# Performance work log

Measured on AMD Instinct MI355X. Metric: run time of the kernel, lower is better.

## Reference

```python
import jax, jax.numpy as jnp
import numpy as np

EPSILON = 1e-10
NUM_STATES = 16
EPS_POT = 1.0
DIFFUSION = 3
N_NODES = 100000
N_UND_EDGES = 1600000
FEAT_DIM = 128


def setup_inputs() -> dict:
    key = jax.random.key(0)
    k1, k2, k3, k4 = jax.random.split(key, 4)
    features = jax.random.normal(k1, (N_NODES, FEAT_DIM), dtype=jnp.float32)
    W = jax.random.normal(k2, (FEAT_DIM, NUM_STATES), dtype=jnp.float32) * 0.05
    u = jax.random.randint(k3, (N_UND_EDGES,), 0, N_NODES)
    v = jax.random.randint(k4, (N_UND_EDGES,), 0, N_NODES)
    # directed edge lists: each undirected edge appears in both directions
    src_nodes = jnp.concatenate([u, v])
    dst_nodes = jnp.concatenate([v, u])
    e = jnp.arange(N_UND_EDGES)
    rev_edges = jnp.concatenate([e + N_UND_EDGES, e])  # index of reversed edge
    return {
        "features": features,
        "W": W,
        "src_nodes": src_nodes,
        "dst_nodes": dst_nodes,
        "rev_edges": rev_edges,
    }


def reference(features, W, src_nodes, dst_nodes, rev_edges):
    num_dir_edges = src_nodes.shape[0]
    potential = jnp.exp(jnp.eye(NUM_STATES, dtype=features.dtype) * EPS_POT)
    # classifier: linear + softmax -> probability priors [N, S]
    priors = jax.nn.softmax(features @ W, axis=1)
    log_priors = jnp.log(jnp.maximum(priors, EPSILON))

    beliefs = priors
    messages = jnp.full((num_dir_edges, NUM_STATES), 1.0 / NUM_STATES,
                        dtype=features.dtype)
    for _ in range(DIFFUSION):
        # message update: gather-divide-matmul-renormalize
        new_beliefs = beliefs[src_nodes]          # [2E, S]
        rev_messages = messages[rev_edges]        # [2E, S]
        new_msgs = (new_beliefs / rev_messages) @ potential
        messages = new_msgs / new_msgs.sum(axis=1, keepdims=True)
        # belief update: scatter-add of log messages, then softmax
        log_msgs = jnp.log(jnp.maximum(messages, EPSILON))
        log_b = log_priors.at[dst_nodes].add(log_msgs)
        beliefs = jax.nn.softmax(log_b, axis=1)
    return (priors, beliefs)
```

## Files before the change

### kernel.cpp

```cpp
#include <hip/hip_runtime.h>
#include <hip/hip_fp16.h>

#define NSTATES 16
#define P_PART 4
#define C_CHUNK 32

static __device__ __forceinline__ float4 ld4(const float* p) {
    return *reinterpret_cast<const float4*>(p);
}

struct h4 { __half2 a, b; };

static __device__ __forceinline__ float4 ldh4(const __half* p) {
    h4 v = *reinterpret_cast<const h4*>(p);
    float2 fa = __half22float2(v.a);
    float2 fb = __half22float2(v.b);
    return make_float4(fa.x, fa.y, fb.x, fb.y);
}
static __device__ __forceinline__ void sth4(__half* p, float4 f) {
    h4 v;
    v.a = __floats2half2_rn(f.x, f.y);
    v.b = __floats2half2_rn(f.z, f.w);
    *reinterpret_cast<h4*>(p) = v;
}

__global__ void priors_kernel(const float* __restrict__ feat,
                              const float* __restrict__ W,
                              float* __restrict__ priors_out,
                              float* __restrict__ beliefs,
                              float* __restrict__ log_priors,
                              int n_nodes)
{
    __shared__ float Wl[128 * NSTATES];
    for (int i = threadIdx.x; i < 128 * NSTATES; i += blockDim.x)
        Wl[i] = W[i];
    __syncthreads();

    long long gid = (long long)blockIdx.x * blockDim.x + threadIdx.x;
    int node = (int)(gid >> 4);
    if (node >= n_nodes) return;
    int s = (int)(gid & 15);

    const float4* f4 = reinterpret_cast<const float4*>(feat + (size_t)node * 128);
    float acc = 0.f;
#pragma unroll
    for (int i = 0; i < 32; ++i) {
        float4 f = f4[i];
        acc = fmaf(f.x, Wl[(i * 4 + 0) * NSTATES + s], acc);
        acc = fmaf(f.y, Wl[(i * 4 + 1) * NSTATES + s], acc);
        acc = fmaf(f.z, Wl[(i * 4 + 2) * NSTATES + s], acc);
        acc = fmaf(f.w, Wl[(i * 4 + 3) * NSTATES + s], acc);
    }
    float mx = acc;
#pragma unroll
    for (int off = 1; off < 16; off <<= 1)
        mx = fmaxf(mx, __shfl_xor(mx, off, 64));
    float ex = expf(acc - mx);
    float sm = ex;
#pragma unroll
    for (int off = 1; off < 16; off <<= 1)
        sm += __shfl_xor(sm, off, 64);
    float p = ex / sm;

    size_t idx = (size_t)node * NSTATES + s;
    priors_out[idx] = p;
    beliefs[idx]    = p;
    log_priors[idx] = logf(fmaxf(p, 1e-10f));
}

__global__ void __launch_bounds__(1024) hist1_kernel(
    const int* __restrict__ dst, int* __restrict__ percount,
    int n, int n_nodes, int bins, int chunk)
{
    extern __shared__ int lh[];
    int c = blockIdx.x & (C_CHUNK - 1);
    int p = blockIdx.x / C_CHUNK;
    int base = p * bins;
    for (int i = threadIdx.x; i < bins; i += 1024) lh[i] = 0;
    __syncthreads();
    int lo = c * chunk, hi = min(lo + chunk, n);
    for (int i = lo + threadIdx.x; i < hi; i += 1024) {
        int d = dst[i] - base;
        if ((unsigned)d < (unsigned)bins) atomicAdd(&lh[d], 1);
    }
    __syncthreads();
    int lim = min(bins, n_nodes - base);
    int* out = percount + (size_t)c * n_nodes + base;
    for (int i = threadIdx.x; i < lim; i += 1024) out[i] = lh[i];
}

__global__ void colscan_kernel(int* __restrict__ percount,
                               int* __restrict__ cnt, int n_nodes)
{
    int v = blockIdx.x * blockDim.x + threadIdx.x;
    if (v >= n_nodes) return;
    int acc = 0;
#pragma unroll
    for (int c = 0; c < C_CHUNK; ++c) {
        size_t idx = (size_t)c * n_nodes + v;
        int x = percount[idx];
        percount[idx] = acc;
        acc += x;
    }
    cnt[v] = acc;
}

__global__ void scan1_kernel(const int* __restrict__ cnt,
                             int* __restrict__ row_ptr,
                             int* __restrict__ bsum, int n)
{
    int base = blockIdx.x * 1024;
    int t = threadIdx.x;
    int i0 = base + t * 4;
    int a0 = (i0 + 0 < n) ? cnt[i0 + 0] : 0;
    int a1 = (i0 + 1 < n) ? cnt[i0 + 1] : 0;
    int a2 = (i0 + 2 < n) ? cnt[i0 + 2] : 0;
    int a3 = (i0 + 3 < n) ? cnt[i0 + 3] : 0;
    int sl = a0 + a1 + a2 + a3;

    int lane = t & 63, wid = t >> 6;
    int v = sl;
#pragma unroll
    for (int off = 1; off < 64; off <<= 1) {
        int tv = __shfl_up(v, off, 64);
        if (lane >= off) v += tv;
    }
    __shared__ int wtot[4], woff[4];
    if (lane == 63) wtot[wid] = v;
    __syncthreads();
    if (t == 0) {
        int a = 0;
        for (int w = 0; w < 4; ++w) { woff[w] = a; a += wtot[w]; }
        bsum[blockIdx.x] = a;
    }
    __syncthreads();
    int excl = woff[wid] + (v - sl);
    if (i0 + 0 < n) row_ptr[i0 + 0] = excl;
    if (i0 + 1 < n) row_ptr[i0 + 1] = excl + a0;
    if (i0 + 2 < n) row_ptr[i0 + 2] = excl + a0 + a1;
    if (i0 + 3 < n) row_ptr[i0 + 3] = excl + a0 + a1 + a2;
}

__global__ void scan2_kernel(int* __restrict__ bsum, int nb)
{
    __shared__ int run;
    int lane = threadIdx.x;
    if (lane == 0) run = 0;
    __syncthreads();
    for (int b = 0; b < nb; b += 64) {
        int i = b + lane;
        int x = (i < nb) ? bsum[i] : 0;
        int v = x;
#pragma unroll
        for (int off = 1; off < 64; off <<= 1) {
            int tv = __shfl_up(v, off, 64);
            if (lane >= off) v += tv;
        }
        int excl = run + v - x;
        if (i < nb) bsum[i] = excl;
        __syncthreads();
        if (lane == 63) run = excl + x;
        __syncthreads();
    }
}

__global__ void scan3_kernel(int* __restrict__ row_ptr,
                             const int* __restrict__ bsum, int n, int total)
{
    int i = blockIdx.x * blockDim.x + threadIdx.x;
    if (i < n) row_ptr[i] += bsum[i >> 10];
    if (i == 0) row_ptr[n] = total;
}

__global__ void __launch_bounds__(1024) slot3_kernel(
    const int* __restrict__ dst, const int* __restrict__ row_ptr,
    const int* __restrict__ percount, int* __restrict__ slot_of,
    int n, int n_nodes, int bins, int chunk)
{
    extern __shared__ int lh[];
    int c = blockIdx.x & (C_CHUNK - 1);
    int p = blockIdx.x / C_CHUNK;
    int base = p * bins;
    for (int i = threadIdx.x; i < bins; i += 1024) lh[i] = 0;
    __syncthreads();
    int lo = c * chunk, hi = min(lo + chunk, n);
    const int* pc = percount + (size_t)c * n_nodes;
    for (int i = lo + threadIdx.x; i < hi; i += 1024) {
        int d = dst[i];
        int ld = d - base;
        if ((unsigned)ld < (unsigned)bins) {
            int lr = atomicAdd(&lh[ld], 1);
            slot_of[i] = row_ptr[d] + pc[d] + lr;
        }
    }
}

template <bool FIRST>
__global__ void edge_kernel(const float* __restrict__ beliefs,
                            __half* __restrict__ messages,
                            const int* __restrict__ src,
                            const int* __restrict__ dst,
                            const int* __restrict__ slot_of,
                            int n_pairs)
{
    long long gid = (long long)blockIdx.x * blockDim.x + threadIdx.x;
    int p = (int)(gid >> 2);
    if (p >= n_pairs) return;
    int sub = (int)(gid & 3);

    int u  = src[p];
    int v  = dst[p];
    int sF = slot_of[p];
    int sR = slot_of[p + n_pairs];

    const float EM1  = 1.7182818284590452354f;
    const float SUMF = 17.718281828459045235f;

    float4 bu = ld4(beliefs + (size_t)u * NSTATES + sub * 4);
    float4 bv = ld4(beliefs + (size_t)v * NSTATES + sub * 4);

    float4 tf, tr;
    if (FIRST) {
        tf = make_float4(bu.x * 16.f, bu.y * 16.f, bu.z * 16.f, bu.w * 16.f);
        tr = make_float4(bv.x * 16.f, bv.y * 16.f, bv.z * 16.f, bv.w * 16.f);
    } else {
        float4 mf = ldh4(messages + (size_t)sF * NSTATES + sub * 4);
        float4 mr = ldh4(messages + (size_t)sR * NSTATES + sub * 4);
        tf = make_float4(bu.x / mr.x, bu.y / mr.y, bu.z / mr.z, bu.w / mr.w);
        tr = make_float4(bv.x / mf.x, bv.y / mf.y, bv.z / mf.z, bv.w / mf.w);
    }

    float sf = (tf.x + tf.y) + (tf.z + tf.w);
    float sr = (tr.x + tr.y) + (tr.z + tr.w);
    sf += __shfl_xor(sf, 1, 64);
    sf += __shfl_xor(sf, 2, 64);
    sr += __shfl_xor(sr, 1, 64);
    sr += __shfl_xor(sr, 2, 64);

    float invf = 1.0f / (SUMF * sf);
    float invr = 1.0f / (SUMF * sr);

    float4 nf, nr;
    nf.x = fmaf(EM1, tf.x, sf) * invf;
    nf.y = fmaf(EM1, tf.y, sf) * invf;
    nf.z = fmaf(EM1, tf.z, sf) * invf;
    nf.w = fmaf(EM1, tf.w, sf) * invf;
    nr.x = fmaf(EM1, tr.x, sr) * invr;
    nr.y = fmaf(EM1, tr.y, sr) * invr;
    nr.z = fmaf(EM1, tr.z, sr) * invr;
    nr.w = fmaf(EM1, tr.w, sr) * invr;

    sth4(messages + (size_t)sF * NSTATES + sub * 4, nf);
    sth4(messages + (size_t)sR * NSTATES + sub * 4, nr);
}

__global__ void belief_kernel(const __half* __restrict__ messages,
                              const int* __restrict__ row_ptr,
                              const float* __restrict__ log_priors,
                              float* __restrict__ beliefs,
                              int n_nodes)
{
    long long gid = (long long)blockIdx.x * blockDim.x + threadIdx.x;
    int node = (int)(gid >> 6);
    if (node >= n_nodes) return;
    int lane = threadIdx.x & 63;
    int cp   = lane & 7;
    int rg   = lane >> 3;

    int start = row_ptr[node];
    int end   = row_ptr[node + 1];

    float acc0 = 0.f, acc1 = 0.f;
    for (int row = start + rg; row < end; row += 8) {
        __half2 m2 = *reinterpret_cast<const __half2*>(
            messages + (size_t)row * NSTATES + cp * 2);
        float2 f = __half22float2(m2);
        acc0 += logf(fmaxf(f.x, 1e-10f));
        acc1 += logf(fmaxf(f.y, 1e-10f));
    }
#pragma unroll
    for (int off = 8; off < 64; off <<= 1) {
        acc0 += __shfl_xor(acc0, off, 64);
        acc1 += __shfl_xor(acc1, off, 64);
    }

    float2 lp = *reinterpret_cast<const float2*>(
        log_priors + (size_t)node * NSTATES + cp * 2);
    float lb0 = acc0 + lp.x;
    float lb1 = acc1 + lp.y;

    float mx = fmaxf(lb0, lb1);
#pragma unroll
    for (int off = 1; off < 8; off <<= 1)
        mx = fmaxf(mx, __shfl_xor(mx, off, 64));
    float e0 = expf(lb0 - mx);
    float e1 = expf(lb1 - mx);
    float sm = e0 + e1;
#pragma unroll
    for (int off = 1; off < 8; off <<= 1)
        sm += __shfl_xor(sm, off, 64);
    float inv = 1.0f / sm;

    if (rg == 0) {
        float2 b = make_float2(e0 * inv, e1 * inv);
        *reinterpret_cast<float2*>(beliefs + (size_t)node * NSTATES + cp * 2) = b;
    }
}

extern "C" void kernel_launch(void* const* d_in, const int* in_sizes, int n_in,
                              void* d_out, int out_size, void* d_ws, size_t ws_size,
                              hipStream_t stream)
{
    const float* feat = (const float*)d_in[0];
    const float* W    = (const float*)d_in[1];
    const int*   src  = (const int*)d_in[2];
    const int*   dst  = (const int*)d_in[3];

    int n_nodes = in_sizes[0] / 128;
    int n_dir   = in_sizes[2];
    int n_pairs = n_dir / 2;

    float* out         = (float*)d_out;
    float* priors_out  = out;
    float* beliefs     = out + (size_t)n_nodes * NSTATES;

    size_t NN16 = (size_t)n_nodes * NSTATES;
    size_t ME   = (size_t)n_dir * NSTATES;

    float*  ws         = (float*)d_ws;
    float*  log_priors = ws;
    __half* messages   = (__half*)(log_priors + NN16);
    int*    slot_of    = (int*)(messages + ME);
    int*    row_ptr    = slot_of + n_dir;
    int*    cnt        = row_ptr + n_nodes + 1;
    int*    bsum       = cnt + n_nodes;
    int*    percount   = bsum + ((n_nodes + 1023) / 1024) + 1;

    const int BLK = 256;
    int nb    = (n_nodes + 1023) / 1024;
    int bins  = (n_nodes + P_PART - 1) / P_PART;
    int chunk = (n_dir + C_CHUNK - 1) / C_CHUNK;
    int grid1 = (int)((NN16 + BLK - 1) / BLK);
    int gridE = (int)(((size_t)n_pairs * 4 + BLK - 1) / BLK);
    int gridN = (n_nodes + BLK - 1) / BLK;
    int gridB = (int)(((size_t)n_nodes * 64 + BLK - 1) / BLK);

    hist1_kernel<<<P_PART * C_CHUNK, 1024, bins * sizeof(int), stream>>>(
        dst, percount, n_dir, n_nodes, bins, chunk);
    colscan_kernel<<<gridN, BLK, 0, stream>>>(percount, cnt, n_nodes);
    scan1_kernel<<<nb, 256, 0, stream>>>(cnt, row_ptr, bsum, n_nodes);
    scan2_kernel<<<1, 64, 0, stream>>>(bsum, nb);
    scan3_kernel<<<gridN, BLK, 0, stream>>>(row_ptr, bsum, n_nodes, n_dir);
    slot3_kernel<<<P_PART * C_CHUNK, 1024, bins * sizeof(int), stream>>>(
        dst, row_ptr, percount, slot_of, n_dir, n_nodes, bins, chunk);

    priors_kernel<<<grid1, BLK, 0, stream>>>(feat, W, priors_out, beliefs,
                                             log_priors, n_nodes);

    edge_kernel<true><<<gridE, BLK, 0, stream>>>(beliefs, messages, src, dst,
                                                 slot_of, n_pairs);
    belief_kernel<<<gridB, BLK, 0, stream>>>(messages, row_ptr, log_priors,
                                             beliefs, n_nodes);

    edge_kernel<false><<<gridE, BLK, 0, stream>>>(beliefs, messages, src, dst,
                                                  slot_of, n_pairs);
    belief_kernel<<<gridB, BLK, 0, stream>>>(messages, row_ptr, log_priors,
                                             beliefs, n_nodes);

    edge_kernel<false><<<gridE, BLK, 0, stream>>>(beliefs, messages, src, dst,
                                                  slot_of, n_pairs);
    belief_kernel<<<gridB, BLK, 0, stream>>>(messages, row_ptr, log_priors,
                                             beliefs, n_nodes);
}
```

Measured before the change: 760.5 us.

## Fuse belief and message updates into a dst-sorted node kernel with reverse-slot map

```diff
diff --git a/kernel.cpp b/kernel.cpp
--- a/kernel.cpp
+++ b/kernel.cpp
@@ -5,30 +5,13 @@
 #define P_PART 4
 #define C_CHUNK 32
 
-static __device__ __forceinline__ float4 ld4(const float* p) {
-    return *reinterpret_cast<const float4*>(p);
-}
-
-struct h4 { __half2 a, b; };
-
-static __device__ __forceinline__ float4 ldh4(const __half* p) {
-    h4 v = *reinterpret_cast<const h4*>(p);
-    float2 fa = __half22float2(v.a);
-    float2 fb = __half22float2(v.b);
-    return make_float4(fa.x, fa.y, fb.x, fb.y);
-}
-static __device__ __forceinline__ void sth4(__half* p, float4 f) {
-    h4 v;
-    v.a = __floats2half2_rn(f.x, f.y);
-    v.b = __floats2half2_rn(f.z, f.w);
-    *reinterpret_cast<h4*>(p) = v;
-}
-
 __global__ void priors_kernel(const float* __restrict__ feat,
                               const float* __restrict__ W,
                               float* __restrict__ priors_out,
-                              float* __restrict__ beliefs,
                               float* __restrict__ log_priors,
+                              const int* __restrict__ srev,
+                              const int* __restrict__ row_ptr,
+                              __half* __restrict__ msgs_out,
                               int n_nodes)
 {
     __shared__ float Wl[128 * NSTATES];
@@ -64,8 +47,18 @@
 
     size_t idx = (size_t)node * NSTATES + s;
     priors_out[idx] = p;
-    beliefs[idx]    = p;
     log_priors[idx] = logf(fmaxf(p, 1e-10f));
+
+    const float EM1  = 1.7182818284590452354f;
+    const float SUMF = 17.718281828459045235f;
+    __half h = __float2half((1.f + EM1 * p) * (1.f / SUMF));
+
+    int start = row_ptr[node];
+    int end   = row_ptr[node + 1];
+    for (int r = start; r < end; ++r) {
+        int tgt = srev[r];
+        msgs_out[(size_t)tgt * NSTATES + s] = h;
+    }
 }
 
 __global__ void __launch_bounds__(1024) hist1_kernel(
@@ -195,115 +188,81 @@
     }
 }
 
-template <bool FIRST>
-__global__ void edge_kernel(const float* __restrict__ beliefs,
-                            __half* __restrict__ messages,
-                            const int* __restrict__ src,
-                            const int* __restrict__ dst,
-                            const int* __restrict__ slot_of,
-                            int n_pairs)
-{
-    long long gid = (long long)blockIdx.x * blockDim.x + threadIdx.x;
-    int p = (int)(gid >> 2);
-    if (p >= n_pairs) return;
-    int sub = (int)(gid & 3);
-
-    int u  = src[p];
-    int v  = dst[p];
-    int sF = slot_of[p];
-    int sR = slot_of[p + n_pairs];
-
-    const float EM1  = 1.7182818284590452354f;
-    const float SUMF = 17.718281828459045235f;
-
-    float4 bu = ld4(beliefs + (size_t)u * NSTATES + sub * 4);
-    float4 bv = ld4(beliefs + (size_t)v * NSTATES + sub * 4);
-
-    float4 tf, tr;
-    if (FIRST) {
-        tf = make_float4(bu.x * 16.f, bu.y * 16.f, bu.z * 16.f, bu.w * 16.f);
-        tr = make_float4(bv.x * 16.f, bv.y * 16.f, bv.z * 16.f, bv.w * 16.f);
-    } else {
-        float4 mf = ldh4(messages + (size_t)sF * NSTATES + sub * 4);
-        float4 mr = ldh4(messages + (size_t)sR * NSTATES + sub * 4);
-        tf = make_float4(bu.x / mr.x, bu.y / mr.y, bu.z / mr.z, bu.w / mr.w);
-        tr = make_float4(bv.x / mf.x, bv.y / mf.y, bv.z / mf.z, bv.w / mf.w);
-    }
-
-    float sf = (tf.x + tf.y) + (tf.z + tf.w);
-    float sr = (tr.x + tr.y) + (tr.z + tr.w);
-    sf += __shfl_xor(sf, 1, 64);
-    sf += __shfl_xor(sf, 2, 64);
-    sr += __shfl_xor(sr, 1, 64);
-    sr += __shfl_xor(sr, 2, 64);
-
-    float invf = 1.0f / (SUMF * sf);
-    float invr = 1.0f / (SUMF * sr);
-
-    float4 nf, nr;
-    nf.x = fmaf(EM1, tf.x, sf) * invf;
-    nf.y = fmaf(EM1, tf.y, sf) * invf;
-    nf.z = fmaf(EM1, tf.z, sf) * invf;
-    nf.w = fmaf(EM1, tf.w, sf) * invf;
-    nr.x = fmaf(EM1, tr.x, sr) * invr;
-    nr.y = fmaf(EM1, tr.y, sr) * invr;
-    nr.z = fmaf(EM1, tr.z, sr) * invr;
-    nr.w = fmaf(EM1, tr.w, sr) * invr;
-
-    sth4(messages + (size_t)sF * NSTATES + sub * 4, nf);
-    sth4(messages + (size_t)sR * NSTATES + sub * 4, nr);
-}
-
-__global__ void belief_kernel(const __half* __restrict__ messages,
-                              const int* __restrict__ row_ptr,
-                              const float* __restrict__ log_priors,
-                              float* __restrict__ beliefs,
-                              int n_nodes)
+__global__ void __launch_bounds__(1024) srev_kernel(
+    const int* __restrict__ slot_of, const int* __restrict__ row_ptr,
+    int* __restrict__ srev, int n, int n_pairs, int n_nodes, int bins, int chunk)
+{
+    int c = blockIdx.x & (C_CHUNK - 1);
+    int p = blockIdx.x / C_CHUNK;
+    int nlo = p * bins;
+    int nhi = min(nlo + bins, n_nodes);
+    int slo = row_ptr[nlo];
+    int shi = row_ptr[nhi];
+    int lo = c * chunk, hi = min(lo + chunk, n);
+    for (int i = lo + threadIdx.x; i < hi; i += 1024) {
+        int s = slot_of[i];
+        if (s >= slo && s < shi) {
+            int r = (i < n_pairs) ? i + n_pairs : i - n_pairs;
+            srev[s] = slot_of[r];
+        }
+    }
+}
+
+template <bool WRITE_MSGS, bool WRITE_B>
+__global__ void fused_kernel(const __half* __restrict__ min_,
+                             __half* __restrict__ mout,
+                             const int* __restrict__ srev,
+                             const int* __restrict__ row_ptr,
+                             const float* __restrict__ log_priors,
+                             float* __restrict__ beliefs_out,
+                             int n_nodes)
 {
     long long gid = (long long)blockIdx.x * blockDim.x + threadIdx.x;
     int node = (int)(gid >> 6);
     if (node >= n_nodes) return;
     int lane = threadIdx.x & 63;
-    int cp   = lane & 7;
-    int rg   = lane >> 3;
+    int j = lane & 15;
+    int g = lane >> 4;
 
     int start = row_ptr[node];
     int end   = row_ptr[node + 1];
 
-    float acc0 = 0.f, acc1 = 0.f;
-    for (int row = start + rg; row < end; row += 8) {
-        __half2 m2 = *reinterpret_cast<const __half2*>(
-            messages + (size_t)row * NSTATES + cp * 2);
-        float2 f = __half22float2(m2);
-        acc0 += logf(fmaxf(f.x, 1e-10f));
-        acc1 += logf(fmaxf(f.y, 1e-10f));
-    }
-#pragma unroll
-    for (int off = 8; off < 64; off <<= 1) {
-        acc0 += __shfl_xor(acc0, off, 64);
-        acc1 += __shfl_xor(acc1, off, 64);
-    }
-
-    float2 lp = *reinterpret_cast<const float2*>(
-        log_priors + (size_t)node * NSTATES + cp * 2);
-    float lb0 = acc0 + lp.x;
-    float lb1 = acc1 + lp.y;
-
-    float mx = fmaxf(lb0, lb1);
-#pragma unroll
-    for (int off = 1; off < 8; off <<= 1)
+    float acc = 0.f;
+    for (int row = start + g; row < end; row += 4)
+        acc += logf(__half2float(min_[(size_t)row * NSTATES + j]));
+    acc += __shfl_xor(acc, 16, 64);
+    acc += __shfl_xor(acc, 32, 64);
+
+    float lb = acc + log_priors[(size_t)node * NSTATES + j];
+    float mx = lb;
+#pragma unroll
+    for (int off = 1; off < 16; off <<= 1)
         mx = fmaxf(mx, __shfl_xor(mx, off, 64));
-    float e0 = expf(lb0 - mx);
-    float e1 = expf(lb1 - mx);
-    float sm = e0 + e1;
-#pragma unroll
-    for (int off = 1; off < 8; off <<= 1)
+    float e_ = expf(lb - mx);
+    float sm = e_;
+#pragma unroll
+    for (int off = 1; off < 16; off <<= 1)
         sm += __shfl_xor(sm, off, 64);
-    float inv = 1.0f / sm;
-
-    if (rg == 0) {
-        float2 b = make_float2(e0 * inv, e1 * inv);
-        *reinterpret_cast<float2*>(beliefs + (size_t)node * NSTATES + cp * 2) = b;
+    float b = e_ / sm;
+
+    if (WRITE_B && g == 0)
+        beliefs_out[(size_t)node * NSTATES + j] = b;
+
+    if (WRITE_MSGS) {
+        const float EM1  = 1.7182818284590452354f;
+        const float SUMF = 17.718281828459045235f;
+        for (int row = start + g; row < end; row += 4) {
+            float m = __half2float(min_[(size_t)row * NSTATES + j]);
+            float t = b / m;
+            float s = t;
+            s += __shfl_xor(s, 1, 64);
+            s += __shfl_xor(s, 2, 64);
+            s += __shfl_xor(s, 4, 64);
+            s += __shfl_xor(s, 8, 64);
+            float out = fmaf(EM1, t, s) * (1.0f / (SUMF * s));
+            int tgt = srev[row];
+            mout[(size_t)tgt * NSTATES + j] = __float2half(out);
+        }
     }
 }
 
@@ -313,7 +272,6 @@
 {
     const float* feat = (const float*)d_in[0];
     const float* W    = (const float*)d_in[1];
-    const int*   src  = (const int*)d_in[2];
     const int*   dst  = (const int*)d_in[3];
 
     int n_nodes = in_sizes[0] / 128;
@@ -322,26 +280,28 @@
 
     float* out         = (float*)d_out;
     float* priors_out  = out;
-    float* beliefs     = out + (size_t)n_nodes * NSTATES;
+    float* beliefs_out = out + (size_t)n_nodes * NSTATES;
 
     size_t NN16 = (size_t)n_nodes * NSTATES;
     size_t ME   = (size_t)n_dir * NSTATES;
 
-    float*  ws         = (float*)d_ws;
-    float*  log_priors = ws;
-    __half* messages   = (__half*)(log_priors + NN16);
-    int*    slot_of    = (int*)(messages + ME);
-    int*    row_ptr    = slot_of + n_dir;
-    int*    cnt        = row_ptr + n_nodes + 1;
-    int*    bsum       = cnt + n_nodes;
-    int*    percount   = bsum + ((n_nodes + 1023) / 1024) + 1;
+    char* base = (char*)d_ws;
+    __half* bufA       = (__half*)base;
+    __half* bufB       = (__half*)(base + ME * sizeof(__half));
+    float*  log_priors = (float*)(base + 2 * ME * sizeof(__half));
+    int*    srev       = (int*)(base + 2 * ME * sizeof(__half) + NN16 * sizeof(float));
+    int*    row_ptr    = srev + n_dir;
+
+    int* cnt      = (int*)bufA;
+    int* bsum     = cnt + n_nodes;
+    int* percount = (int*)bufB;
+    int* slot_of  = percount + (size_t)C_CHUNK * n_nodes;
 
     const int BLK = 256;
     int nb    = (n_nodes + 1023) / 1024;
     int bins  = (n_nodes + P_PART - 1) / P_PART;
     int chunk = (n_dir + C_CHUNK - 1) / C_CHUNK;
     int grid1 = (int)((NN16 + BLK - 1) / BLK);
-    int gridE = (int)(((size_t)n_pairs * 4 + BLK - 1) / BLK);
     int gridN = (n_nodes + BLK - 1) / BLK;
     int gridB = (int)(((size_t)n_nodes * 64 + BLK - 1) / BLK);
 
@@ -353,22 +313,16 @@
     scan3_kernel<<<gridN, BLK, 0, stream>>>(row_ptr, bsum, n_nodes, n_dir);
     slot3_kernel<<<P_PART * C_CHUNK, 1024, bins * sizeof(int), stream>>>(
         dst, row_ptr, percount, slot_of, n_dir, n_nodes, bins, chunk);
-
-    priors_kernel<<<grid1, BLK, 0, stream>>>(feat, W, priors_out, beliefs,
-                                             log_priors, n_nodes);
-
-    edge_kernel<true><<<gridE, BLK, 0, stream>>>(beliefs, messages, src, dst,
-                                                 slot_of, n_pairs);
-    belief_kernel<<<gridB, BLK, 0, stream>>>(messages, row_ptr, log_priors,
-                                             beliefs, n_nodes);
-
-    edge_kernel<false><<<gridE, BLK, 0, stream>>>(beliefs, messages, src, dst,
-                                                  slot_of, n_pairs);
-    belief_kernel<<<gridB, BLK, 0, stream>>>(messages, row_ptr, log_priors,
-                                             beliefs, n_nodes);
-
-    edge_kernel<false><<<gridE, BLK, 0, stream>>>(beliefs, messages, src, dst,
-                                                  slot_of, n_pairs);
-    belief_kernel<<<gridB, BLK, 0, stream>>>(messages, row_ptr, log_priors,
-                                             beliefs, n_nodes);
-}
+    srev_kernel<<<P_PART * C_CHUNK, 1024, 0, stream>>>(
+        slot_of, row_ptr, srev, n_dir, n_pairs, n_nodes, bins, chunk);
+
+    priors_kernel<<<grid1, BLK, 0, stream>>>(feat, W, priors_out, log_priors,
+                                             srev, row_ptr, bufA, n_nodes);
+
+    fused_kernel<true, false><<<gridB, BLK, 0, stream>>>(
+        bufA, bufB, srev, row_ptr, log_priors, nullptr, n_nodes);
+    fused_kernel<true, false><<<gridB, BLK, 0, stream>>>(
+        bufB, bufA, srev, row_ptr, log_priors, nullptr, n_nodes);
+    fused_kernel<false, true><<<gridB, BLK, 0, stream>>>(
+        bufA, nullptr, nullptr, row_ptr, log_priors, beliefs_out, n_nodes);
+}
```

Result: faster. 691.4 us (-9.1%).
